# Performance work log

Hardware: AMD Instinct MI355X
Metric: run time of the kernel (lower is better)

Reference implementation:

```python
import jax, jax.numpy as jnp
import numpy as np

N_NODES = 50000
N_EDGES = 400000
DIMS = 32
HEADS = 6
FEAT = DIMS * HEADS  # 192
NEG_SLOPE = 0.2  # PyG GATv2Conv default


def glorot(key, shape):
    fan_in, fan_out = shape[0], shape[1]
    lim = jnp.sqrt(6.0 / (fan_in + fan_out))
    return jax.random.uniform(key, shape, jnp.float32, -lim, lim)


def setup_inputs() -> dict:
    key = jax.random.key(0)
    ks = jax.random.split(key, 10)
    x = jax.random.normal(ks[0], (N_NODES, FEAT), jnp.float32)
    edge_index = jax.random.randint(ks[1], (2, N_EDGES), 0, N_NODES, jnp.int32)
    edge_weights = jax.random.uniform(ks[2], (N_EDGES, 1), jnp.float32)
    W_l = glorot(ks[3], (FEAT, FEAT))   # lin_l: in -> heads*out
    b_l = jnp.zeros((FEAT,), jnp.float32)
    W_r = glorot(ks[4], (FEAT, FEAT))   # lin_r (share_weights=False)
    b_r = jnp.zeros((FEAT,), jnp.float32)
    W_edge = glorot(ks[5], (1, FEAT))   # lin_edge: edge_dim=1 -> heads*out, no bias
    att = glorot(ks[6], (HEADS, DIMS))  # attention vector per head
    bias = jnp.zeros((FEAT,), jnp.float32)
    return {"x": x, "edge_index": edge_index, "edge_weights": edge_weights,
            "W_l": W_l, "b_l": b_l, "W_r": W_r, "b_r": b_r,
            "W_edge": W_edge, "att": att, "bias": bias}


def gatv2_res(x, edge_index, edge_weights, W_l, b_l, W_r, b_r, W_edge, att, bias):
    N = x.shape[0]
    H, C = att.shape
    src0, dst0 = edge_index[0], edge_index[1]

    # add_self_loops with fill_value='mean': self-loop attr = mean of edge_attr over incoming edges
    cnt = jax.ops.segment_sum(jnp.ones((edge_weights.shape[0],), x.dtype), dst0, num_segments=N)
    loop_attr = jax.ops.segment_sum(edge_weights, dst0, num_segments=N) / jnp.maximum(cnt, 1.0)[:, None]
    loops = jnp.arange(N, dtype=src0.dtype)
    src = jnp.concatenate([src0, loops])
    dst = jnp.concatenate([dst0, loops])
    e_attr = jnp.concatenate([edge_weights, loop_attr], axis=0)  # [E+N, 1]

    x_l = (x @ W_l + b_l).reshape(N, H, C)  # source transform
    x_r = (x @ W_r + b_r).reshape(N, H, C)  # target transform
    e_emb = (e_attr @ W_edge).reshape(-1, H, C)

    # per-edge GATv2 score
    m = jax.nn.leaky_relu(x_l[src] + x_r[dst] + e_emb, NEG_SLOPE)  # [E+N, H, C]
    alpha = jnp.einsum('ehc,hc->eh', m, att)  # [E+N, H]

    # segment softmax over edges incident to each target node (self-loops guarantee coverage)
    amax = jax.lax.stop_gradient(jax.ops.segment_max(alpha, dst, num_segments=N))
    ex = jnp.exp(alpha - amax[dst])
    denom = jax.ops.segment_sum(ex, dst, num_segments=N)
    a = ex / denom[dst]  # [E+N, H]

    out = jax.ops.segment_sum(x_l[src] * a[..., None], dst, num_segments=N)  # [N, H, C]
    out = out.reshape(N, H * C) + bias

    # ResLayer: residual + ReLU (dropout = identity in eval mode)
    return jax.nn.relu(x + out)


def reference(x, edge_index, edge_weights, W_l, b_l, W_r, b_r, W_edge, att, bias):
    return gatv2_res(x, edge_index, edge_weights, W_l, b_l, W_r, b_r, W_edge, att, bias)
```

## Files before the change

### kernel.cpp

```cpp
#include <hip/hip_runtime.h>
#include <hip/hip_bf16.h>
#include <math.h>

#define N_NODES 50000
#define N_EDGES 400000
#define HEADS 6
#define DIMS 32
#define FEAT 192
#define NEG_SLOPE 0.2f

typedef __attribute__((ext_vector_type(8))) short short8;
typedef __attribute__((ext_vector_type(4))) float f32x4;

__device__ __forceinline__ unsigned short f2bu(float f) {
    __hip_bfloat16 h = __float2bfloat16(f);
    unsigned short u; __builtin_memcpy(&u, &h, 2); return u;
}
__device__ __forceinline__ float bu2f(unsigned short u) {
    return __uint_as_float(((unsigned)u) << 16);
}

#define XL_OFF    0
#define XR_OFF    19200000
#define WT_OFF    38400000
#define BLR_OFF   38547456
#define PAIR_OFF  38548992
#define DEG_OFF   41748992
#define WSUM_OFF  41948992
#define SCAN_OFF  42148992
#define BSUM_OFF  42348992
#define BOFF_OFF  42350016
#define NB_SCAN ((N_NODES + 255) / 256)

__global__ __launch_bounds__(256) void k_count(const int* __restrict__ ei,
                                               const float* __restrict__ ew,
                                               int* __restrict__ deg,
                                               float* __restrict__ wsum,
                                               const float* __restrict__ Wl,
                                               const float* __restrict__ Wr,
                                               const float* __restrict__ bl,
                                               const float* __restrict__ br,
                                               short* __restrict__ Wt,
                                               float* __restrict__ blr) {
    int e = blockIdx.x * blockDim.x + threadIdx.x;
    if (e < N_EDGES) {
        int d = ei[N_EDGES + e];
        atomicAdd(&deg[d], 1);
        unsafeAtomicAdd(&wsum[d], ew[e]);
    }
    if (e < 384 * FEAT) {
        int n = e / FEAT, k = e - n * FEAT;
        float v = (n < FEAT) ? Wl[k * FEAT + n] : Wr[k * FEAT + (n - FEAT)];
        Wt[n * FEAT + k] = (short)f2bu(v);
    }
    if (e < 384) blr[e] = (e < FEAT) ? bl[e] : br[e - FEAT];
}

__global__ __launch_bounds__(256) void k_scan1(const int* __restrict__ deg,
                                               int* __restrict__ scan,
                                               int* __restrict__ bsums) {
    int t = threadIdx.x;
    int i = blockIdx.x * 256 + t;
    int v = (i < N_NODES) ? deg[i] : 0;
    __shared__ int s[256];
    s[t] = v; __syncthreads();
    for (int off = 1; off < 256; off <<= 1) {
        int u = (t >= off) ? s[t - off] : 0;
        __syncthreads();
        s[t] += u;
        __syncthreads();
    }
    if (i < N_NODES) scan[i] = s[t];
    if (t == 255) bsums[blockIdx.x] = s[255];
}

__global__ __launch_bounds__(256) void k_scan2(int* __restrict__ bsums,
                                               int* __restrict__ boffs) {
    int t = threadIdx.x;
    int v = (t < NB_SCAN) ? bsums[t] : 0;
    __shared__ int s[256];
    s[t] = v; __syncthreads();
    for (int off = 1; off < 256; off <<= 1) {
        int u = (t >= off) ? s[t - off] : 0;
        __syncthreads();
        s[t] += u;
        __syncthreads();
    }
    boffs[t] = s[t] - v;
}

#define SCAT_BLOCKS ((N_EDGES + 383) / 384)
#define GEMM_BLOCKS (N_NODES / 16)
#define OSTRIDE 392
#define ASTRIDE 200
__global__ __launch_bounds__(384) void k_scatgemm(const int* __restrict__ ei,
                                                  const float* __restrict__ ew,
                                                  const int* __restrict__ scan,
                                                  const int* __restrict__ boffs,
                                                  int* __restrict__ deg,
                                                  int2* __restrict__ pair,
                                                  const float* __restrict__ x,
                                                  const short* __restrict__ Wt,
                                                  const float* __restrict__ blr,
                                                  unsigned short* __restrict__ xl,
                                                  unsigned short* __restrict__ xr) {
    __shared__ unsigned short sOut[16 * OSTRIDE];
    __shared__ unsigned short sA[16 * ASTRIDE];
    if (blockIdx.x < SCAT_BLOCKS) {
        int e = blockIdx.x * 384 + threadIdx.x;
        if (e < N_EDGES) {
            int d = ei[N_EDGES + e];
            int inclEnd = boffs[d >> 8] + scan[d];
            int old = atomicSub(&deg[d], 1);
            int2 p; p.x = ei[e]; p.y = __float_as_int(ew[e]);
            pair[inclEnd - old] = p;
        }
        return;
    }
    size_t row0 = (size_t)(blockIdx.x - SCAT_BLOCKS) * 16;

    {
        int q = threadIdx.x;
        int row = q / 24, k0 = (q - row * 24) * 8;
        const float* ap = x + (row0 + row) * FEAT + k0;
        float4 v0 = *(const float4*)ap;
        float4 v1 = *(const float4*)(ap + 4);
        unsigned short tmp[8];
        tmp[0] = f2bu(v0.x); tmp[1] = f2bu(v0.y); tmp[2] = f2bu(v0.z); tmp[3] = f2bu(v0.w);
        tmp[4] = f2bu(v1.x); tmp[5] = f2bu(v1.y); tmp[6] = f2bu(v1.z); tmp[7] = f2bu(v1.w);
        int kw = (k0 >> 1) ^ ((row & 7) << 2);
        *(uint4*)&sA[row * ASTRIDE + kw * 2] = *(const uint4*)tmp;
    }
    __syncthreads();

    int wv   = threadIdx.x >> 6;
    int lane = threadIdx.x & 63;
    int m    = lane & 15;
    int kg   = lane >> 4;
    int ncol0 = wv * 64;

    f32x4 acc0 = {0.f,0.f,0.f,0.f}, acc1 = acc0, acc2 = acc0, acc3 = acc0;

#pragma unroll
    for (int ks = 0; ks < 6; ks++) {
        int kb = ks * 32 + kg * 8;
        int kw = (kb >> 1) ^ ((m & 7) << 2);
        short8 af = *(const short8*)&sA[m * ASTRIDE + kw * 2];
        const short* wp = Wt + (size_t)(ncol0 + m) * FEAT + kb;
        short8 b0 = *(const short8*)(wp);
        short8 b1 = *(const short8*)(wp + 16 * FEAT);
        short8 b2 = *(const short8*)(wp + 32 * FEAT);
        short8 b3 = *(const short8*)(wp + 48 * FEAT);
        acc0 = __builtin_amdgcn_mfma_f32_16x16x32_bf16(af, b0, acc0, 0, 0, 0);
        acc1 = __builtin_amdgcn_mfma_f32_16x16x32_bf16(af, b1, acc1, 0, 0, 0);
        acc2 = __builtin_amdgcn_mfma_f32_16x16x32_bf16(af, b2, acc2, 0, 0, 0);
        acc3 = __builtin_amdgcn_mfma_f32_16x16x32_bf16(af, b3, acc3, 0, 0, 0);
    }

    f32x4 accs[4] = {acc0, acc1, acc2, acc3};
#pragma unroll
    for (int t4 = 0; t4 < 4; t4++) {
        int cc = ncol0 + t4 * 16 + m;
        float bv = blr[cc];
#pragma unroll
        for (int r = 0; r < 4; r++) {
            sOut[(kg * 4 + r) * OSTRIDE + cc] = f2bu(accs[t4][r] + bv);
        }
    }
    __syncthreads();
    for (int q = threadIdx.x; q < 768; q += 384) {
        int row = q / 48, p = q - row * 48;
        uint4 v = *(const uint4*)&sOut[row * OSTRIDE + p * 8];
        if (p < 24) *(uint4*)(xl + (row0 + row) * FEAT + p * 8) = v;
        else        *(uint4*)(xr + (row0 + row) * FEAT + (p - 24) * 8) = v;
    }
}

#define NPB 8
#define CEDGE 32
#define RS 100
#define APAD 36
__global__ __launch_bounds__(192) void k_node(const float* __restrict__ x,
                                              const float* __restrict__ bias,
                                              const float* __restrict__ att,
                                              const float* __restrict__ We,
                                              const int* __restrict__ scan,
                                              const int* __restrict__ boffs,
                                              const float* __restrict__ wsum,
                                              const int2* __restrict__ pair,
                                              const unsigned short* __restrict__ xl,
                                              const unsigned short* __restrict__ xr,
                                              float* __restrict__ out) {
    __shared__ __align__(16) unsigned int sXL[CEDGE * RS];
    __shared__ __align__(16) unsigned int sXR[NPB * RS];
    __shared__ float sEx[CEDGE * HEADS];
    __shared__ float sExS[NPB * HEADS];
    __shared__ int   sSrc[2][CEDGE];
    __shared__ float sW[2][CEDGE];
    __shared__ int   sDst[2][CEDGE];
    __shared__ int   sStart[NPB + 1];
    __shared__ __align__(16) float sAttP[HEADS * APAD];
    __shared__ __align__(16) float sWeP[HEADS * APAD];
    __shared__ float sDen[NPB * HEADS];

    int t = threadIdx.x;
    int h = t >> 5;
    int n0 = blockIdx.x * NPB;

    int gbase = boffs[n0 >> 8] + ((n0 & 255) ? scan[n0 - 1] : 0);
    int n8 = n0 + NPB;
    int gend = (n8 >= N_NODES) ? N_EDGES
             : (boffs[n8 >> 8] + ((n8 & 255) ? scan[n8 - 1] : 0));
    int etot = gend - gbase;
    int c0 = min(etot, CEDGE);

    if (t < c0) { int2 p = pair[gbase + t]; sSrc[0][t] = p.x; sW[0][t] = __int_as_float(p.y); }

    for (int q = t; q < HEADS * APAD; q += 192) {
        int hh = q / APAD, c = q - hh * APAD;
        if (c < 32) { sAttP[q] = att[hh * 32 + c]; sWeP[q] = We[hh * 32 + c]; }
    }
    if (t <= NPB) {
        int n = n0 + t;
        int st;
        if (n >= N_NODES) st = N_EDGES;
        else {
            int b = n >> 8;
            st = boffs[b] + ((n & 255) ? scan[n - 1] : 0);
        }
        sStart[t] = st;
    }
    if (t < NPB) {
        int n = n0 + t;
        int a = boffs[n >> 8] + ((n & 255) ? scan[n - 1] : 0);
        int n1 = n + 1;
        int b = (n1 >= N_NODES) ? N_EDGES
              : (boffs[n1 >> 8] + ((n1 & 255) ? scan[n1 - 1] : 0));
        int lo = a - gbase; if (lo < 0) lo = 0;
        int hi = b - gbase; if (hi > c0) hi = c0;
        for (int q = lo; q < hi; q++) sDst[0][q] = t;
    }
    {
        int nn = t / 24, p = t - nn * 24;
        *(uint4*)&sXR[nn * RS + p * 4] = ((const uint4*)(xr + (size_t)(n0 + nn) * FEAT))[p];
    }
    __syncthreads();

    float acc[NPB];
#pragma unroll
    for (int nn = 0; nn < NPB; nn++) acc[nn] = 0.f;
    float denR = 0.f;
    int nnD = t / HEADS, hhD = t - nnD * HEADS;

    int nch = (etot + CEDGE - 1) / CEDGE;
    for (int ci = 0; ci < nch; ci++) {
        int i0 = ci * CEDGE;
        int c  = min(etot - i0, CEDGE);
        int cn = min(etot - i0 - CEDGE, CEDGE);
        int cb = ci & 1, nb = cb ^ 1;

        {
            int nld = c * 24;
#pragma unroll
            for (int s = 0; s < 4; s++) {
                int q = t + s * 192;
                if (q < nld) {
                    int i = q / 24, p = q - i * 24;
                    *(uint4*)&sXL[i * RS + p * 4] =
                        *(const uint4*)(xl + (size_t)sSrc[cb][i] * FEAT + p * 8);
                }
            }
        }
        int2 P;
        if (t < cn) P = pair[gbase + i0 + CEDGE + t];
        if (t < NPB && cn > 0) {
            int lo = sStart[t] - gbase - i0 - CEDGE;     if (lo < 0) lo = 0;
            int hi = sStart[t + 1] - gbase - i0 - CEDGE; if (hi > cn) hi = cn;
            for (int q = lo; q < hi; q++) sDst[nb][q] = t;
        }
        __syncthreads();

        if (t < c * HEADS) {
            int i = t / HEADS, hh = t - i * HEADS;
            int nn = sDst[cb][i];
            float w = sW[cb][i];
            const uint4* pa = (const uint4*)&sXL[i * RS + hh * 16];
            const uint4* pb = (const uint4*)&sXR[nn * RS + hh * 16];
            float alpha = 0.f;
#pragma unroll
            for (int g = 0; g < 4; g++) {
                uint4 a4 = pa[g];
                uint4 b4 = pb[g];
                float4 we0 = *(const float4*)&sWeP[hh * APAD + g * 8];
                float4 we1 = *(const float4*)&sWeP[hh * APAD + g * 8 + 4];
                float4 at0 = *(const float4*)&sAttP[hh * APAD + g * 8];
                float4 at1 = *(const float4*)&sAttP[hh * APAD + g * 8 + 4];
                float wec[8] = {we0.x, we0.y, we0.z, we0.w, we1.x, we1.y, we1.z, we1.w};
                float atc[8] = {at0.x, at0.y, at0.z, at0.w, at1.x, at1.y, at1.z, at1.w};
                unsigned aw[4] = {a4.x, a4.y, a4.z, a4.w};
                unsigned bw[4] = {b4.x, b4.y, b4.z, b4.w};
#pragma unroll
                for (int q = 0; q < 4; q++) {
                    float m0 = bu2f((unsigned short)aw[q]) + bu2f((unsigned short)bw[q]) + w * wec[q * 2];
                    m0 = fmaxf(m0, NEG_SLOPE * m0);
                    alpha += m0 * atc[q * 2];
                    float m1 = bu2f((unsigned short)(aw[q] >> 16)) + bu2f((unsigned short)(bw[q] >> 16)) + w * wec[q * 2 + 1];
                    m1 = fmaxf(m1, NEG_SLOPE * m1);
                    alpha += m1 * atc[q * 2 + 1];
                }
            }
            sEx[t] = __expf(alpha);
        }
        if (t < cn) { sSrc[nb][t] = P.x; sW[nb][t] = __int_as_float(P.y); }
        __syncthreads();

        {
            int cw = t >> 1;
#pragma unroll
            for (int nn = 0; nn < NPB; nn++) {
                int lo = sStart[nn] - gbase - i0;     if (lo < 0) lo = 0;
                int hi = sStart[nn + 1] - gbase - i0; if (hi > c) hi = c;
                for (int i = lo; i < hi; i++) {
                    float ex = sEx[i * HEADS + h];
                    unsigned u = sXL[i * RS + cw];
                    unsigned short v = (t & 1) ? (unsigned short)(u >> 16) : (unsigned short)u;
                    acc[nn] += ex * bu2f(v);
                }
            }
            if (t < NPB * HEADS) {
                int lo = sStart[nnD] - gbase - i0;     if (lo < 0) lo = 0;
                int hi = sStart[nnD + 1] - gbase - i0; if (hi > c) hi = c;
                for (int i = lo; i < hi; i++) denR += sEx[i * HEADS + hhD];
            }
        }
        __syncthreads();
    }

    if (t < NPB * HEADS) {
        sDen[t] = denR;
        int nn = nnD, hh = hhD;
        int dg = sStart[nn + 1] - sStart[nn];
        float w = wsum[n0 + nn] / fmaxf((float)dg, 1.0f);
        const uint4* pa = (const uint4*)(xl + (size_t)(n0 + nn) * FEAT + hh * 32);
        const uint4* pb = (const uint4*)&sXR[nn * RS + hh * 16];
        float alpha = 0.f;
#pragma unroll
        for (int g = 0; g < 4; g++) {
            uint4 a4 = pa[g];
            uint4 b4 = pb[g];
            float4 we0 = *(const float4*)&sWeP[hh * APAD + g * 8];
            float4 we1 = *(const float4*)&sWeP[hh * APAD + g * 8 + 4];
            float4 at0 = *(const float4*)&sAttP[hh * APAD + g * 8];
            float4 at1 = *(const float4*)&sAttP[hh * APAD + g * 8 + 4];
            float wec[8] = {we0.x, we0.y, we0.z, we0.w, we1.x, we1.y, we1.z, we1.w};
            float atc[8] = {at0.x, at0.y, at0.z, at0.w, at1.x, at1.y, at1.z, at1.w};
            unsigned aw[4] = {a4.x, a4.y, a4.z, a4.w};
            unsigned bw[4] = {b4.x, b4.y, b4.z, b4.w};
#pragma unroll
            for (int q = 0; q < 4; q++) {
                float m0 = bu2f((unsigned short)aw[q]) + bu2f((unsigned short)bw[q]) + w * wec[q * 2];
                m0 = fmaxf(m0, NEG_SLOPE * m0);
                alpha += m0 * atc[q * 2];
                float m1 = bu2f((unsigned short)(aw[q] >> 16)) + bu2f((unsigned short)(bw[q] >> 16)) + w * wec[q * 2 + 1];
                m1 = fmaxf(m1, NEG_SLOPE * m1);
                alpha += m1 * atc[q * 2 + 1];
            }
        }
        sExS[t] = __expf(alpha);
    }
    __syncthreads();

    float bj = bias[t];
#pragma unroll
    for (int nn = 0; nn < NPB; nn++) {
        float exS = sExS[nn * HEADS + h];
        size_t off = (size_t)(n0 + nn) * FEAT + t;
        float xsv = bu2f(xl[off]);
        float num = acc[nn] + exS * xsv;
        float dn  = sDen[nn * HEADS + h] + exS;
        float val = x[off] + bj + num / dn;
        out[off] = (val > 0.f) ? val : 0.f;
    }
}

extern "C" void kernel_launch(void* const* d_in, const int* in_sizes, int n_in,
                              void* d_out, int out_size, void* d_ws, size_t ws_size,
                              hipStream_t stream) {
    const float* x    = (const float*)d_in[0];
    const int*   ei   = (const int*)d_in[1];
    const float* ew   = (const float*)d_in[2];
    const float* Wl   = (const float*)d_in[3];
    const float* bl   = (const float*)d_in[4];
    const float* Wr   = (const float*)d_in[5];
    const float* br   = (const float*)d_in[6];
    const float* We   = (const float*)d_in[7];
    const float* att  = (const float*)d_in[8];
    const float* bias = (const float*)d_in[9];
    float* out = (float*)d_out;

    char* ws = (char*)d_ws;
    unsigned short* xl = (unsigned short*)(ws + XL_OFF);
    unsigned short* xr = (unsigned short*)(ws + XR_OFF);
    short* Wt     = (short*)(ws + WT_OFF);
    float* blr    = (float*)(ws + BLR_OFF);
    int2*  pair   = (int2*)(ws + PAIR_OFF);
    int*   deg    = (int*)(ws + DEG_OFF);
    float* wsum   = (float*)(ws + WSUM_OFF);
    int*   scan   = (int*)(ws + SCAN_OFF);
    int*   bsums  = (int*)(ws + BSUM_OFF);
    int*   boffs  = (int*)(ws + BOFF_OFF);

    hipMemsetAsync(ws + DEG_OFF, 0, 2 * N_NODES * sizeof(int), stream);

    k_count<<<(N_EDGES + 255) / 256, 256, 0, stream>>>(ei, ew, deg, wsum, Wl, Wr, bl, br, Wt, blr);
    k_scan1<<<NB_SCAN, 256, 0, stream>>>(deg, scan, bsums);
    k_scan2<<<1, 256, 0, stream>>>(bsums, boffs);

    k_scatgemm<<<SCAT_BLOCKS + GEMM_BLOCKS, 384, 0, stream>>>(ei, ew, scan, boffs, deg,
                                                              pair, x, Wt, blr, xl, xr);

    k_node<<<N_NODES / NPB, 192, 0, stream>>>(x, bias, att, We, scan, boffs, wsum,
                                              pair, xl, xr, out);
}
```

Baseline: 305.2 us.

## Aggregate per-node edge messages with bf16 MFMA using one-hot ownership matrices

The per-thread scalar loops that accumulated ex·x_l for each destination node, and the attention denominators, are replaced by 16x16x32 bf16 MFMA calls. A one-hot matrix mapping each edge to its destination node, scaled by the edge's exp score, multiplies the gathered x_l chunk, and a ones operand gives the denominators. Scores are split into hi/lo bf16 parts to keep near-fp32 accuracy, which doubles the MFMA count. Results are staged through shared memory (reusing the x_l buffer) before the final epilogue. Building the operands needs extra shared-memory reads and conversions, and only 8 of the 16 MFMA rows are used.

```diff
diff --git a/kernel.cpp b/kernel.cpp
--- a/kernel.cpp
+++ b/kernel.cpp
@@ -180,6 +180,7 @@
 #define CEDGE 32
 #define RS 100
 #define APAD 36
+#define ACS 196
 __global__ __launch_bounds__(192) void k_node(const float* __restrict__ x,
                                               const float* __restrict__ bias,
                                               const float* __restrict__ att,
@@ -205,6 +206,8 @@
 
     int t = threadIdx.x;
     int h = t >> 5;
+    int lane = t & 63;
+    int wv = t >> 6;
     int n0 = blockIdx.x * NPB;
 
     int gbase = boffs[n0 >> 8] + ((n0 & 255) ? scan[n0 - 1] : 0);
@@ -246,10 +249,12 @@
     }
     __syncthreads();
 
-    float acc[NPB];
-#pragma unroll
-    for (int nn = 0; nn < NPB; nn++) acc[nn] = 0.f;
-    float denR = 0.f;
+    f32x4 zz = {0.f,0.f,0.f,0.f};
+    f32x4 cA0 = zz, cA1 = zz, cB0 = zz, cB1 = zz, dA = zz, dB = zz;
+    short8 kOnes;
+#pragma unroll
+    for (int j = 0; j < 8; j++) kOnes[j] = (short)0x3F80;
+
     int nnD = t / HEADS, hhD = t - nnD * HEADS;
 
     int nch = (etot + CEDGE - 1) / CEDGE;
@@ -315,29 +320,70 @@
         __syncthreads();
 
         {
-            int cw = t >> 1;
-#pragma unroll
-            for (int nn = 0; nn < NPB; nn++) {
-                int lo = sStart[nn] - gbase - i0;     if (lo < 0) lo = 0;
-                int hi = sStart[nn + 1] - gbase - i0; if (hi > c) hi = c;
-                for (int i = lo; i < hi; i++) {
-                    float ex = sEx[i * HEADS + h];
-                    unsigned u = sXL[i * RS + cw];
-                    unsigned short v = (t & 1) ? (unsigned short)(u >> 16) : (unsigned short)u;
-                    acc[nn] += ex * bu2f(v);
+            const unsigned short* xlu = (const unsigned short*)sXL;
+            int g8 = (lane >> 4) * 8;
+            int r  = lane & 15;
+#pragma unroll
+            for (int hid = 0; hid < 2; hid++) {
+                int hh = wv * 2 + hid;
+                short8 aHi, aLo, b0, b1;
+#pragma unroll
+                for (int j = 0; j < 8; j++) {
+                    int i = g8 + j;
+                    bool ok = (i < c);
+                    float ex = ok ? sEx[i * HEADS + hh] : 0.f;
+                    int dd = sDst[cb][i];
+                    unsigned short exHi = f2bu(ex);
+                    unsigned short exLo = f2bu(ex - bu2f(exHi));
+                    bool own = ok && (dd == r);
+                    aHi[j] = own ? (short)exHi : (short)0;
+                    aLo[j] = own ? (short)exLo : (short)0;
+                    int ub = i * (RS * 2) + hh * 32 + r;
+                    b0[j] = ok ? (short)xlu[ub] : (short)0;
+                    b1[j] = ok ? (short)xlu[ub + 16] : (short)0;
+                }
+                if (hid == 0) {
+                    cA0 = __builtin_amdgcn_mfma_f32_16x16x32_bf16(aHi, b0, cA0, 0, 0, 0);
+                    cA0 = __builtin_amdgcn_mfma_f32_16x16x32_bf16(aLo, b0, cA0, 0, 0, 0);
+                    cA1 = __builtin_amdgcn_mfma_f32_16x16x32_bf16(aHi, b1, cA1, 0, 0, 0);
+                    cA1 = __builtin_amdgcn_mfma_f32_16x16x32_bf16(aLo, b1, cA1, 0, 0, 0);
+                    dA  = __builtin_amdgcn_mfma_f32_16x16x32_bf16(aHi, kOnes, dA, 0, 0, 0);
+                    dA  = __builtin_amdgcn_mfma_f32_16x16x32_bf16(aLo, kOnes, dA, 0, 0, 0);
+                } else {
+                    cB0 = __builtin_amdgcn_mfma_f32_16x16x32_bf16(aHi, b0, cB0, 0, 0, 0);
+                    cB0 = __builtin_amdgcn_mfma_f32_16x16x32_bf16(aLo, b0, cB0, 0, 0, 0);
+                    cB1 = __builtin_amdgcn_mfma_f32_16x16x32_bf16(aHi, b1, cB1, 0, 0, 0);
+                    cB1 = __builtin_amdgcn_mfma_f32_16x16x32_bf16(aLo, b1, cB1, 0, 0, 0);
+                    dB  = __builtin_amdgcn_mfma_f32_16x16x32_bf16(aHi, kOnes, dB, 0, 0, 0);
+                    dB  = __builtin_amdgcn_mfma_f32_16x16x32_bf16(aLo, kOnes, dB, 0, 0, 0);
                 }
             }
-            if (t < NPB * HEADS) {
-                int lo = sStart[nnD] - gbase - i0;     if (lo < 0) lo = 0;
-                int hi = sStart[nnD + 1] - gbase - i0; if (hi > c) hi = c;
-                for (int i = lo; i < hi; i++) denR += sEx[i * HEADS + hhD];
+        }
+        __syncthreads();
+    }
+
+    {
+        float* sAcc = (float*)sXL;
+        int rowg = lane >> 4;
+        int cc   = lane & 15;
+        if (rowg < 2) {
+#pragma unroll
+            for (int rg = 0; rg < 4; rg++) {
+                int nn = rowg * 4 + rg;
+                int h0 = wv * 2, h1 = wv * 2 + 1;
+                sAcc[nn * ACS + h0 * 32 + cc]      = cA0[rg];
+                sAcc[nn * ACS + h0 * 32 + 16 + cc] = cA1[rg];
+                sAcc[nn * ACS + h1 * 32 + cc]      = cB0[rg];
+                sAcc[nn * ACS + h1 * 32 + 16 + cc] = cB1[rg];
+                if (cc == 0) {
+                    sDen[nn * HEADS + h0] = dA[rg];
+                    sDen[nn * HEADS + h1] = dB[rg];
+                }
             }
         }
-        __syncthreads();
     }
 
     if (t < NPB * HEADS) {
-        sDen[t] = denR;
         int nn = nnD, hh = hhD;
         int dg = sStart[nn + 1] - sStart[nn];
         float w = wsum[n0 + nn] / fmaxf((float)dg, 1.0f);
@@ -370,16 +416,22 @@
     }
     __syncthreads();
 
-    float bj = bias[t];
-#pragma unroll
-    for (int nn = 0; nn < NPB; nn++) {
-        float exS = sExS[nn * HEADS + h];
-        size_t off = (size_t)(n0 + nn) * FEAT + t;
-        float xsv = bu2f(xl[off]);
-        float num = acc[nn] + exS * xsv;
-        float dn  = sDen[nn * HEADS + h] + exS;
-        float val = x[off] + bj + num / dn;
-        out[off] = (val > 0.f) ? val : 0.f;
+    {
+        const float* sAcc = (const float*)sXL;
+        float bj = bias[t];
+        float accv[NPB];
+#pragma unroll
+        for (int nn = 0; nn < NPB; nn++) accv[nn] = sAcc[nn * ACS + t];
+#pragma unroll
+        for (int nn = 0; nn < NPB; nn++) {
+            float exS = sExS[nn * HEADS + h];
+            size_t off = (size_t)(n0 + nn) * FEAT + t;
+            float xsv = bu2f(xl[off]);
+            float num = accv[nn] + exS * xsv;
+            float dn  = sDen[nn * HEADS + h] + exS;
+            float val = x[off] + bj + num / dn;
+            out[off] = (val > 0.f) ? val : 0.f;
+        }
     }
 }
 
```

Result: slower. 312.4 us (+2.4%).

## Compute self-loop weight mean in node kernel and widen node blocks to 16

Applied to the files above, without the earlier changes.

Removes the float atomic accumulation of edge weights per destination in the counting kernel. Instead, each node block sums the weights from its already-loaded CSR edge chunks in shared memory. The node kernel also grows from 8 to 16 nodes per block and from 32 to 64 edges per chunk, using 384 threads split into two 192-thread groups of 8 nodes each. This cuts atomic traffic and a workspace buffer, and amortises per-block setup, at the cost of more shared memory per block and fewer, larger blocks.

```diff
diff --git a/kernel.cpp b/kernel.cpp
--- a/kernel.cpp
+++ b/kernel.cpp
@@ -26,16 +26,13 @@
 #define BLR_OFF   38547456
 #define PAIR_OFF  38548992
 #define DEG_OFF   41748992
-#define WSUM_OFF  41948992
 #define SCAN_OFF  42148992
 #define BSUM_OFF  42348992
 #define BOFF_OFF  42350016
 #define NB_SCAN ((N_NODES + 255) / 256)
 
 __global__ __launch_bounds__(256) void k_count(const int* __restrict__ ei,
-                                               const float* __restrict__ ew,
                                                int* __restrict__ deg,
-                                               float* __restrict__ wsum,
                                                const float* __restrict__ Wl,
                                                const float* __restrict__ Wr,
                                                const float* __restrict__ bl,
@@ -43,11 +40,7 @@
                                                short* __restrict__ Wt,
                                                float* __restrict__ blr) {
     int e = blockIdx.x * blockDim.x + threadIdx.x;
-    if (e < N_EDGES) {
-        int d = ei[N_EDGES + e];
-        atomicAdd(&deg[d], 1);
-        unsafeAtomicAdd(&wsum[d], ew[e]);
-    }
+    if (e < N_EDGES) atomicAdd(&deg[ei[N_EDGES + e]], 1);
     if (e < 384 * FEAT) {
         int n = e / FEAT, k = e - n * FEAT;
         float v = (n < FEAT) ? Wl[k * FEAT + n] : Wr[k * FEAT + (n - FEAT)];
@@ -176,17 +169,16 @@
     }
 }
 
-#define NPB 8
-#define CEDGE 32
+#define NPB 16
+#define CEDGE 64
 #define RS 100
 #define APAD 36
-__global__ __launch_bounds__(192) void k_node(const float* __restrict__ x,
+__global__ __launch_bounds__(384) void k_node(const float* __restrict__ x,
                                               const float* __restrict__ bias,
                                               const float* __restrict__ att,
                                               const float* __restrict__ We,
                                               const int* __restrict__ scan,
                                               const int* __restrict__ boffs,
-                                              const float* __restrict__ wsum,
                                               const int2* __restrict__ pair,
                                               const unsigned short* __restrict__ xl,
                                               const unsigned short* __restrict__ xr,
@@ -202,21 +194,21 @@
     __shared__ __align__(16) float sAttP[HEADS * APAD];
     __shared__ __align__(16) float sWeP[HEADS * APAD];
     __shared__ float sDen[NPB * HEADS];
+    __shared__ float sWsm[NPB];
 
     int t = threadIdx.x;
-    int h = t >> 5;
     int n0 = blockIdx.x * NPB;
 
     int gbase = boffs[n0 >> 8] + ((n0 & 255) ? scan[n0 - 1] : 0);
-    int n8 = n0 + NPB;
-    int gend = (n8 >= N_NODES) ? N_EDGES
-             : (boffs[n8 >> 8] + ((n8 & 255) ? scan[n8 - 1] : 0));
+    int n16 = n0 + NPB;
+    int gend = (n16 >= N_NODES) ? N_EDGES
+             : (boffs[n16 >> 8] + ((n16 & 255) ? scan[n16 - 1] : 0));
     int etot = gend - gbase;
     int c0 = min(etot, CEDGE);
 
     if (t < c0) { int2 p = pair[gbase + t]; sSrc[0][t] = p.x; sW[0][t] = __int_as_float(p.y); }
 
-    for (int q = t; q < HEADS * APAD; q += 192) {
+    for (int q = t; q < HEADS * APAD; q += 384) {
         int hh = q / APAD, c = q - hh * APAD;
         if (c < 32) { sAttP[q] = att[hh * 32 + c]; sWeP[q] = We[hh * 32 + c]; }
     }
@@ -246,10 +238,15 @@
     }
     __syncthreads();
 
-    float acc[NPB];
-#pragma unroll
-    for (int nn = 0; nn < NPB; nn++) acc[nn] = 0.f;
-    float denR = 0.f;
+    float acc[8];
+#pragma unroll
+    for (int nn = 0; nn < 8; nn++) acc[nn] = 0.f;
+    float denR = 0.f, wsP = 0.f;
+    int grp  = t / 192;
+    int ch   = t - grp * 192;
+    int h    = ch >> 5;
+    int cw   = ch >> 1;
+    int base = grp * 8;
     int nnD = t / HEADS, hhD = t - nnD * HEADS;
 
     int nch = (etot + CEDGE - 1) / CEDGE;
@@ -263,7 +260,7 @@
             int nld = c * 24;
 #pragma unroll
             for (int s = 0; s < 4; s++) {
-                int q = t + s * 192;
+                int q = t + s * 384;
                 if (q < nld) {
                     int i = q / 24, p = q - i * 24;
                     *(uint4*)&sXL[i * RS + p * 4] =
@@ -315,15 +312,14 @@
         __syncthreads();
 
         {
-            int cw = t >> 1;
-#pragma unroll
-            for (int nn = 0; nn < NPB; nn++) {
-                int lo = sStart[nn] - gbase - i0;     if (lo < 0) lo = 0;
-                int hi = sStart[nn + 1] - gbase - i0; if (hi > c) hi = c;
+#pragma unroll
+            for (int nn = 0; nn < 8; nn++) {
+                int lo = sStart[base + nn] - gbase - i0;     if (lo < 0) lo = 0;
+                int hi = sStart[base + nn + 1] - gbase - i0; if (hi > c) hi = c;
                 for (int i = lo; i < hi; i++) {
                     float ex = sEx[i * HEADS + h];
                     unsigned u = sXL[i * RS + cw];
-                    unsigned short v = (t & 1) ? (unsigned short)(u >> 16) : (unsigned short)u;
+                    unsigned short v = (ch & 1) ? (unsigned short)(u >> 16) : (unsigned short)u;
                     acc[nn] += ex * bu2f(v);
                 }
             }
@@ -331,16 +327,24 @@
                 int lo = sStart[nnD] - gbase - i0;     if (lo < 0) lo = 0;
                 int hi = sStart[nnD + 1] - gbase - i0; if (hi > c) hi = c;
                 for (int i = lo; i < hi; i++) denR += sEx[i * HEADS + hhD];
+            } else if (t < NPB * HEADS + NPB) {
+                int nw = t - NPB * HEADS;
+                int lo = sStart[nw] - gbase - i0;     if (lo < 0) lo = 0;
+                int hi = sStart[nw + 1] - gbase - i0; if (hi > c) hi = c;
+                for (int i = lo; i < hi; i++) wsP += sW[cb][i];
             }
         }
         __syncthreads();
     }
 
+    if (t < NPB * HEADS) sDen[t] = denR;
+    else if (t < NPB * HEADS + NPB) sWsm[t - NPB * HEADS] = wsP;
+    __syncthreads();
+
     if (t < NPB * HEADS) {
-        sDen[t] = denR;
         int nn = nnD, hh = hhD;
         int dg = sStart[nn + 1] - sStart[nn];
-        float w = wsum[n0 + nn] / fmaxf((float)dg, 1.0f);
+        float w = sWsm[nn] / fmaxf((float)dg, 1.0f);
         const uint4* pa = (const uint4*)(xl + (size_t)(n0 + nn) * FEAT + hh * 32);
         const uint4* pb = (const uint4*)&sXR[nn * RS + hh * 16];
         float alpha = 0.f;
@@ -370,16 +374,19 @@
     }
     __syncthreads();
 
-    float bj = bias[t];
-#pragma unroll
-    for (int nn = 0; nn < NPB; nn++) {
-        float exS = sExS[nn * HEADS + h];
-        size_t off = (size_t)(n0 + nn) * FEAT + t;
-        float xsv = bu2f(xl[off]);
-        float num = acc[nn] + exS * xsv;
-        float dn  = sDen[nn * HEADS + h] + exS;
-        float val = x[off] + bj + num / dn;
-        out[off] = (val > 0.f) ? val : 0.f;
+    {
+        float bj = bias[ch];
+#pragma unroll
+        for (int nn = 0; nn < 8; nn++) {
+            int ln = base + nn;
+            float exS = sExS[ln * HEADS + h];
+            size_t off = (size_t)(n0 + ln) * FEAT + ch;
+            float xsv = bu2f(xl[off]);
+            float num = acc[nn] + exS * xsv;
+            float dn  = sDen[ln * HEADS + h] + exS;
+            float val = x[off] + bj + num / dn;
+            out[off] = (val > 0.f) ? val : 0.f;
+        }
     }
 }
 
@@ -405,20 +412,19 @@
     float* blr    = (float*)(ws + BLR_OFF);
     int2*  pair   = (int2*)(ws + PAIR_OFF);
     int*   deg    = (int*)(ws + DEG_OFF);
-    float* wsum   = (float*)(ws + WSUM_OFF);
     int*   scan   = (int*)(ws + SCAN_OFF);
     int*   bsums  = (int*)(ws + BSUM_OFF);
     int*   boffs  = (int*)(ws + BOFF_OFF);
 
-    hipMemsetAsync(ws + DEG_OFF, 0, 2 * N_NODES * sizeof(int), stream);
-
-    k_count<<<(N_EDGES + 255) / 256, 256, 0, stream>>>(ei, ew, deg, wsum, Wl, Wr, bl, br, Wt, blr);
+    hipMemsetAsync(ws + DEG_OFF, 0, N_NODES * sizeof(int), stream);
+
+    k_count<<<(N_EDGES + 255) / 256, 256, 0, stream>>>(ei, deg, Wl, Wr, bl, br, Wt, blr);
     k_scan1<<<NB_SCAN, 256, 0, stream>>>(deg, scan, bsums);
     k_scan2<<<1, 256, 0, stream>>>(bsums, boffs);
 
     k_scatgemm<<<SCAT_BLOCKS + GEMM_BLOCKS, 384, 0, stream>>>(ei, ew, scan, boffs, deg,
                                                               pair, x, Wt, blr, xl, xr);
 
-    k_node<<<N_NODES / NPB, 192, 0, stream>>>(x, bias, att, We, scan, boffs, wsum,
+    k_node<<<N_NODES / NPB, 384, 0, stream>>>(x, bias, att, We, scan, boffs,
                                               pair, xl, xr, out);
 }
```

Result: slower. 339.2 us (+11.2%).
